# Kernel optimization log

Measured on AMD Instinct MI355X. Metric: run time of the kernel, lower is better.

## Reference

```python
import jax, jax.numpy as jnp
import numpy as np

VOCAB = 32000
EMB = 512
STATE = 512
B = 4
S = 1024


def setup_inputs() -> dict:
    key = jax.random.key(0)
    ks = jax.random.split(key, 6)
    x = jax.random.randint(ks[0], (B, S), 0, VOCAB)
    emb_table = jax.random.normal(ks[1], (VOCAB, EMB), dtype=jnp.float32)
    a = jax.random.normal(ks[2], (STATE, STATE), dtype=jnp.float32) * 0.02
    b = jax.random.normal(ks[3], (EMB, STATE), dtype=jnp.float32) * 0.02
    # nn.Linear(state, vocab): weight [vocab, state], bias [vocab]
    lim = 1.0 / np.sqrt(STATE)
    c_w = jax.random.uniform(ks[4], (VOCAB, STATE), minval=-lim, maxval=lim, dtype=jnp.float32)
    c_b = jax.random.uniform(ks[5], (VOCAB,), minval=-lim, maxval=lim, dtype=jnp.float32)
    return {"x": x, "emb_table": emb_table, "a": a, "b": b, "c_w": c_w, "c_b": c_b}


def reference(x, emb_table, a, b, c_w, c_b):
    emb = emb_table[x]                      # [B, S, E]
    # Precompute input projection for all timesteps (single GEMM).
    u = jnp.einsum('bse,en->bsn', emb, b)   # [B, S, N]
    u_t = jnp.swapaxes(u, 0, 1)             # [S, B, N] for scan

    def step(state, u_step):
        new_state = jnp.tanh(state @ a + u_step)  # [B, N]
        return new_state, new_state

    init = jnp.zeros((x.shape[0], a.shape[0]), dtype=emb.dtype)
    _, states = jax.lax.scan(step, init, u_t)   # states: [S, B, N]
    # Readout (dropout=0 -> identity). One big GEMM over all timesteps.
    logits = jnp.einsum('sbn,vn->sbv', states, c_w) + c_b  # [S, B, V]
    return jnp.swapaxes(logits, 0, 1)           # [B, S, V]
```

## Files before the change

### kernel.cpp

```cpp
#include <hip/hip_runtime.h>
#include <hip/hip_fp16.h>

typedef _Float16 f16;
typedef _Float16 f16x8 __attribute__((ext_vector_type(8)));
typedef _Float16 f16x4 __attribute__((ext_vector_type(4)));
typedef float f32x4v __attribute__((ext_vector_type(4)));
typedef unsigned long long u64;

#define S_LEN 1024
#define NS 512
#define NV 32000
#define NW 4
#define SENT 0x7C007C007C007C00ULL
#define FUSED_LDS 98304
#define TPB 896

#define MFMA16(a, b, c) __builtin_amdgcn_mfma_f32_16x16x32_f16((a), (b), (c), 0, 0, 0)

#define XLD(p) __hip_atomic_load((p), __ATOMIC_RELAXED, __HIP_MEMORY_SCOPE_AGENT)


__global__ __launch_bounds__(256) void transpose512_f16_kernel(
        const float* __restrict__ src, f16* __restrict__ dstT,
        u64* __restrict__ X) {
    int idx = blockIdx.x * 256 + threadIdx.x;
    X[idx] = SENT;
    X[idx + 262144] = SENT;
    int r = idx >> 9;
    int c = idx & 511;
    dstT[c * 512 + r] = (f16)src[idx];
}

__global__ __launch_bounds__(256) void embu_kernel(
        const int* __restrict__ x, const float* __restrict__ emb,
        const f16* __restrict__ bT, f16* __restrict__ u16) {
    __shared__ f16 embA[64 * 40];
    __shared__ f16 Bt[512 * 40];
    __shared__ int xi[64];

    int t = threadIdx.x;
    int wg = blockIdx.x;
    if (t < 64) {
        int m = wg * 64 + t;
        int bb = m & 3, ss = m >> 2;
        xi[t] = x[bb * S_LEN + ss];
    }
    __syncthreads();

    int wv = t >> 6, l = t & 63, lr = l & 15, lg = l >> 4;

    f32x4v acc[32];
#pragma unroll
    for (int i = 0; i < 32; i++) acc[i] = (f32x4v){0.f, 0.f, 0.f, 0.f};

    for (int kc = 0; kc < 512; kc += 32) {
        __syncthreads();
        {
            int tk = t >> 2, c0 = (t & 3) * 8;
            const float* src = emb + (size_t)xi[tk] * NS + kc + c0;
            float4 v0 = *(const float4*)src;
            float4 v1 = *(const float4*)(src + 4);
            f16x8 h;
            h[0] = (f16)v0.x; h[1] = (f16)v0.y; h[2] = (f16)v0.z; h[3] = (f16)v0.w;
            h[4] = (f16)v1.x; h[5] = (f16)v1.y; h[6] = (f16)v1.z; h[7] = (f16)v1.w;
            *(f16x8*)&embA[tk * 40 + c0] = h;
        }
        {
            int c0 = (t & 3) * 8;
            int n0 = t >> 2;
#pragma unroll
            for (int rr = 0; rr < 8; rr++) {
                int n = rr * 64 + n0;
                f16x8 v = *(const f16x8*)&bT[n * 512 + kc + c0];
                *(f16x8*)&Bt[n * 40 + c0] = v;
            }
        }
        __syncthreads();

        f16x8 af = *(const f16x8*)&embA[(wv * 16 + lr) * 40 + 8 * lg];
#pragma unroll
        for (int vt = 0; vt < 32; vt++) {
            f16x8 bf = *(const f16x8*)&Bt[(vt * 16 + lr) * 40 + 8 * lg];
            acc[vt] = MFMA16(af, bf, acc[vt]);
        }
    }

    int m0 = wg * 64 + wv * 16 + 4 * lg;
    int ss = m0 >> 2;
#pragma unroll
    for (int vt = 0; vt < 32; vt++) {
        int n = vt * 16 + lr;
        f16x4 h;
#pragma unroll
        for (int i = 0; i < 4; i++) h[i] = (f16)acc[vt][i];
        *(f16x4*)&u16[((size_t)ss * NS + n) * 4] = h;
    }
}

__global__ __launch_bounds__(TPB) void fused_kernel(
        const float* __restrict__ a, const f16* __restrict__ u16,
        const float* __restrict__ cw, const float* __restrict__ cb,
        u64* __restrict__ X, float* __restrict__ out) {
    extern __shared__ char smem[];
    int t = threadIdx.x;
    int bid = blockIdx.x;
    int w = t >> 6, l = t & 63, lr = l & 15, lg = l >> 4;

    if (bid < NW) {
        f16* Sb = (f16*)smem;
        int r = bid;

        for (int i = t; i < 2 * 4 * 544; i += TPB) Sb[i] = (f16)0.f;

        if (w < 8) {
            int col = r * 128 + w * 16 + lr;

            f16x8 afr[16];
#pragma unroll
            for (int ks = 0; ks < 16; ks++) {
                f16x8 h;
#pragma unroll
                for (int j = 0; j < 8; j++)
                    h[j] = (f16)a[(size_t)(ks * 32 + 8 * lg + j) * NS + col];
                afr[ks] = h;
            }

            f16x4 upf = *(const f16x4*)&u16[(size_t)col * 4];

            __syncthreads();

#pragma unroll 1
            for (int s = 0; s < S_LEN; s++) {
                int cur = s & 1, nxt = cur ^ 1;

                f32x4v acca, accb;
                acca[0] = (float)upf[0]; acca[1] = (float)upf[1];
                acca[2] = (float)upf[2]; acca[3] = (float)upf[3];
                accb = (f32x4v){0.f, 0.f, 0.f, 0.f};

                {
                    int sn = (s + 1 < S_LEN) ? s + 1 : S_LEN - 1;
                    upf = *(const f16x4*)&u16[((size_t)sn * NS + col) * 4];
                }

                const char* sb = (const char*)Sb + cur * 4352 +
                                 (lr & 3) * 1088 + lg * 16;
#pragma unroll
                for (int ks = 0; ks < 16; ks += 2) {
                    f16x8 s0 = *(const f16x8*)(sb + ks * 64);
                    f16x8 s1 = *(const f16x8*)(sb + ks * 64 + 64);
                    acca = MFMA16(s0, afr[ks], acca);
                    accb = MFMA16(s1, afr[ks + 1], accb);
                }

                if (lg == 0) {
                    union { u64 u; f16 h[4]; } pk;
#pragma unroll
                    for (int i = 0; i < 4; i++) {
                        float y = acca[i] + accb[i];
                        float e = __expf(2.0f * y);
                        float rc = __builtin_amdgcn_rcpf(e + 1.0f);
                        y = __builtin_fmaf(-2.0f, rc, 1.0f);
                        pk.h[i] = (f16)y;
                    }
                    __hip_atomic_store(&X[(size_t)s * NS + col], pk.u,
                                       __ATOMIC_RELAXED,
                                       __HIP_MEMORY_SCOPE_AGENT);
                    if (s < S_LEN - 1) {
#pragma unroll
                        for (int i = 0; i < 4; i++)
                            Sb[nxt * 2176 + i * 544 + col] = pk.h[i];
                    }
                }
                if (s == S_LEN - 1) break;

                asm volatile("s_waitcnt lgkmcnt(0)" ::: "memory");
                __builtin_amdgcn_s_barrier();
                __builtin_amdgcn_sched_barrier(0);
            }
        } else {
            int gw = w - 8;
            int cwk = gw + (gw >= 2 * r ? 2 : 0);
            int gcol = cwk * 64 + l;

            __syncthreads();

#pragma unroll 1
            for (int s = 0; s < S_LEN - 1; s++) {
                int nxt = (s & 1) ^ 1;
                const u64* p = &X[(size_t)s * NS + gcol];

                u64 v;
                u64 a0 = XLD(p), a1 = XLD(p), a2 = XLD(p), a3 = XLD(p);
                for (;;) {
                    if (a0 != SENT) { v = a0; break; }
                    a0 = XLD(p);
                    if (a1 != SENT) { v = a1; break; }
                    a1 = XLD(p);
                    if (a2 != SENT) { v = a2; break; }
                    a2 = XLD(p);
                    if (a3 != SENT) { v = a3; break; }
                    a3 = XLD(p);
                }
                __builtin_amdgcn_sched_barrier(0);

                union { u64 u; f16 h[4]; } pk;
                pk.u = v;
#pragma unroll
                for (int i = 0; i < 4; i++)
                    Sb[nxt * 2176 + i * 544 + gcol] = pk.h[i];

                asm volatile("s_waitcnt lgkmcnt(0)" ::: "memory");
                __builtin_amdgcn_s_barrier();
                __builtin_amdgcn_sched_barrier(0);
            }
        }
        return;
    }

    char* AstB = smem;
    char* BwB  = smem + 256 * 64 * 2;

    int idx = bid - NW;
    int bm = idx / 250;
    int bn = idx % 250;
    int s0 = bm * 64;

    if (t == 0) {
        int sc = s0 + 56;
        while (XLD(&X[(size_t)sc * NS]) == SENT)
            __builtin_amdgcn_s_sleep(16);
    }
    __syncthreads();

    int wr = w >> 1, wc = w & 1;

    f32x4v acc[4][4];
#pragma unroll
    for (int i = 0; i < 4; i++)
#pragma unroll
        for (int j = 0; j < 4; j++) acc[i][j] = (f32x4v){0.f, 0.f, 0.f, 0.f};

    for (int kc = 0; kc < 512; kc += 64) {
        __syncthreads();
        if (t < 512) {
            {
                int srel = t >> 3;
                int ck = (t & 7) * 8;
                const u64* xs = &X[(size_t)(s0 + srel) * NS + kc + ck];
                u64 v[8];
#pragma unroll
                for (int j = 0; j < 8; j++) v[j] = xs[j];
#pragma unroll
                for (int j = 0; j < 8; j++)
                    while (v[j] == SENT) v[j] = XLD(&xs[j]);
#pragma unroll
                for (int b = 0; b < 4; b++) {
                    f16x8 row;
#pragma unroll
                    for (int j = 0; j < 8; j++) {
                        union { u64 u; f16 h[4]; } pk;
                        pk.u = v[j];
                        row[j] = pk.h[b];
                    }
                    int rr = srel * 4 + b;
                    int byte = (rr * 128 + ck * 2) ^ ((rr & 7) << 4);
                    *(f16x8*)(AstB + byte) = row;
                }
            }
#pragma unroll
            for (int q = 0; q < 4; q++) {
                int i2 = q * 512 + t;
                int row = i2 >> 4;
                int c0 = (i2 & 15) * 4;
                float4 v = *(const float4*)&cw[(size_t)(bn * 128 + row) * NS +
                                               kc + c0];
                f16x4 h;
                h[0] = (f16)v.x; h[1] = (f16)v.y; h[2] = (f16)v.z; h[3] = (f16)v.w;
                int byte = (row * 128 + c0 * 2) ^ ((row & 7) << 4);
                *(f16x4*)(BwB + byte) = h;
            }
        }
        __syncthreads();

        if (w < 8) {
#pragma unroll
            for (int ks = 0; ks < 2; ks++) {
                f16x8 af[4], bf[4];
#pragma unroll
                for (int mt = 0; mt < 4; mt++) {
                    int rr = wr * 64 + mt * 16 + lr;
                    int byte = (rr * 128 + ks * 64 + lg * 16) ^ ((lr & 7) << 4);
                    af[mt] = *(const f16x8*)(AstB + byte);
                }
#pragma unroll
                for (int vt = 0; vt < 4; vt++) {
                    int rr = wc * 64 + vt * 16 + lr;
                    int byte = (rr * 128 + ks * 64 + lg * 16) ^ ((lr & 7) << 4);
                    bf[vt] = *(const f16x8*)(BwB + byte);
                }
#pragma unroll
                for (int mt = 0; mt < 4; mt++)
#pragma unroll
                    for (int vt = 0; vt < 4; vt++)
                        acc[mt][vt] = MFMA16(af[mt], bf[vt], acc[mt][vt]);
            }
        }
    }

    if (w < 8) {
        float bias[4];
#pragma unroll
        for (int vt = 0; vt < 4; vt++)
            bias[vt] = cb[bn * 128 + wc * 64 + vt * 16 + lr];

#pragma unroll
        for (int mt = 0; mt < 4; mt++) {
#pragma unroll
            for (int i = 0; i < 4; i++) {
                int m = bm * 256 + wr * 64 + mt * 16 + 4 * lg + i;
                int bb = m & 3, ss = m >> 2;
                float* orow = out + (size_t)(bb * S_LEN + ss) * NV +
                              bn * 128 + wc * 64;
#pragma unroll
                for (int vt = 0; vt < 4; vt++)
                    orow[vt * 16 + lr] = acc[mt][vt][i] + bias[vt];
            }
        }
    }
}

extern "C" void kernel_launch(void* const* d_in, const int* in_sizes, int n_in,
                              void* d_out, int out_size, void* d_ws, size_t ws_size,
                              hipStream_t stream) {
    (void)in_sizes; (void)n_in; (void)out_size; (void)ws_size;

    const int*   x   = (const int*)d_in[0];
    const float* emb = (const float*)d_in[1];
    const float* a   = (const float*)d_in[2];
    const float* bm  = (const float*)d_in[3];
    const float* cw  = (const float*)d_in[4];
    const float* cb  = (const float*)d_in[5];
    float* out = (float*)d_out;

    char* ws = (char*)d_ws;
    f16* u16 = (f16*)(ws);
    u64* X   = (u64*)(ws + (4u << 20));
    f16* bT16 = (f16*)(ws + (8u << 20));

    hipFuncSetAttribute(reinterpret_cast<const void*>(fused_kernel),
                        hipFuncAttributeMaxDynamicSharedMemorySize,
                        FUSED_LDS);

    transpose512_f16_kernel<<<1024, 256, 0, stream>>>(bm, bT16, X);
    embu_kernel<<<64, 256, 0, stream>>>(x, emb, bT16, u16);
    fused_kernel<<<NW + 16 * 250, TPB, FUSED_LDS, stream>>>(
        a, u16, cw, cb, X, out);
}
```

Before: 1.462 ms.

## Shrink fused kernel to 512 threads and merge gather role into compute waves

The block size drops from 896 to 512 threads. The dedicated gather waves (waves 8-13) of the recurrence blocks are removed, so six of the eight compute waves now also poll the global X buffer for other blocks' state columns after each step. The GEMM blocks no longer carry six idle waves, which can raise occupancy and register budget per thread. The cost is that polling now sits on the critical path of the compute waves in the serial recurrence, which could lengthen every step.

Measured after the change: 1.486 ms. Within noise of the previous version (+1.6%).

```diff
diff --git a/kernel.cpp b/kernel.cpp
--- a/kernel.cpp
+++ b/kernel.cpp
@@ -13,7 +13,6 @@
 #define NW 4
 #define SENT 0x7C007C007C007C00ULL
 #define FUSED_LDS 98304
-#define TPB 896
 
 #define MFMA16(a, b, c) __builtin_amdgcn_mfma_f32_16x16x32_f16((a), (b), (c), 0, 0, 0)
 
@@ -97,7 +96,7 @@
     }
 }
 
-__global__ __launch_bounds__(TPB) void fused_kernel(
+__global__ __launch_bounds__(512) void fused_kernel(
         const float* __restrict__ a, const f16* __restrict__ u16,
         const float* __restrict__ cw, const float* __restrict__ cb,
         u64* __restrict__ X, float* __restrict__ out) {
@@ -109,87 +108,75 @@
     if (bid < NW) {
         f16* Sb = (f16*)smem;
         int r = bid;
-
-        for (int i = t; i < 2 * 4 * 544; i += TPB) Sb[i] = (f16)0.f;
-
-        if (w < 8) {
-            int col = r * 128 + w * 16 + lr;
-
-            f16x8 afr[16];
-#pragma unroll
-            for (int ks = 0; ks < 16; ks++) {
-                f16x8 h;
-#pragma unroll
-                for (int j = 0; j < 8; j++)
-                    h[j] = (f16)a[(size_t)(ks * 32 + 8 * lg + j) * NS + col];
-                afr[ks] = h;
-            }
-
-            f16x4 upf = *(const f16x4*)&u16[(size_t)col * 4];
-
-            __syncthreads();
+        int col = r * 128 + w * 16 + lr;
+
+        int gcol = -1;
+        if (w < 6) {
+            int cwk = w + (w >= 2 * r ? 2 : 0);
+            gcol = cwk * 64 + l;
+        }
+
+        for (int i = t; i < 2 * 4 * 544; i += 512) Sb[i] = (f16)0.f;
+
+        f16x8 afr[16];
+#pragma unroll
+        for (int ks = 0; ks < 16; ks++) {
+            f16x8 h;
+#pragma unroll
+            for (int j = 0; j < 8; j++)
+                h[j] = (f16)a[(size_t)(ks * 32 + 8 * lg + j) * NS + col];
+            afr[ks] = h;
+        }
+
+        f16x4 upf = *(const f16x4*)&u16[(size_t)col * 4];
+
+        __syncthreads();
 
 #pragma unroll 1
-            for (int s = 0; s < S_LEN; s++) {
-                int cur = s & 1, nxt = cur ^ 1;
-
-                f32x4v acca, accb;
-                acca[0] = (float)upf[0]; acca[1] = (float)upf[1];
-                acca[2] = (float)upf[2]; acca[3] = (float)upf[3];
-                accb = (f32x4v){0.f, 0.f, 0.f, 0.f};
-
-                {
-                    int sn = (s + 1 < S_LEN) ? s + 1 : S_LEN - 1;
-                    upf = *(const f16x4*)&u16[((size_t)sn * NS + col) * 4];
+        for (int s = 0; s < S_LEN; s++) {
+            int cur = s & 1, nxt = cur ^ 1;
+
+            f32x4v acca, accb;
+            acca[0] = (float)upf[0]; acca[1] = (float)upf[1];
+            acca[2] = (float)upf[2]; acca[3] = (float)upf[3];
+            accb = (f32x4v){0.f, 0.f, 0.f, 0.f};
+
+            {
+                int sn = (s + 1 < S_LEN) ? s + 1 : S_LEN - 1;
+                upf = *(const f16x4*)&u16[((size_t)sn * NS + col) * 4];
+            }
+
+            const char* sb = (const char*)Sb + cur * 4352 +
+                             (lr & 3) * 1088 + lg * 16;
+#pragma unroll
+            for (int ks = 0; ks < 16; ks += 2) {
+                f16x8 s0 = *(const f16x8*)(sb + ks * 64);
+                f16x8 s1 = *(const f16x8*)(sb + ks * 64 + 64);
+                acca = MFMA16(s0, afr[ks], acca);
+                accb = MFMA16(s1, afr[ks + 1], accb);
+            }
+
+            if (lg == 0) {
+                union { u64 u; f16 h[4]; } pk;
+#pragma unroll
+                for (int i = 0; i < 4; i++) {
+                    float y = acca[i] + accb[i];
+                    float e = __expf(2.0f * y);
+                    float rc = __builtin_amdgcn_rcpf(e + 1.0f);
+                    y = __builtin_fmaf(-2.0f, rc, 1.0f);
+                    pk.h[i] = (f16)y;
                 }
-
-                const char* sb = (const char*)Sb + cur * 4352 +
-                                 (lr & 3) * 1088 + lg * 16;
-#pragma unroll
-                for (int ks = 0; ks < 16; ks += 2) {
-                    f16x8 s0 = *(const f16x8*)(sb + ks * 64);
-                    f16x8 s1 = *(const f16x8*)(sb + ks * 64 + 64);
-                    acca = MFMA16(s0, afr[ks], acca);
-                    accb = MFMA16(s1, afr[ks + 1], accb);
-                }
-
-                if (lg == 0) {
-                    union { u64 u; f16 h[4]; } pk;
-#pragma unroll
-                    for (int i = 0; i < 4; i++) {
-                        float y = acca[i] + accb[i];
-                        float e = __expf(2.0f * y);
-                        float rc = __builtin_amdgcn_rcpf(e + 1.0f);
-                        y = __builtin_fmaf(-2.0f, rc, 1.0f);
-                        pk.h[i] = (f16)y;
-                    }
-                    __hip_atomic_store(&X[(size_t)s * NS + col], pk.u,
-                                       __ATOMIC_RELAXED,
-                                       __HIP_MEMORY_SCOPE_AGENT);
-                    if (s < S_LEN - 1) {
-#pragma unroll
-                        for (int i = 0; i < 4; i++)
-                            Sb[nxt * 2176 + i * 544 + col] = pk.h[i];
-                    }
-                }
-                if (s == S_LEN - 1) break;
-
-                asm volatile("s_waitcnt lgkmcnt(0)" ::: "memory");
-                __builtin_amdgcn_s_barrier();
-                __builtin_amdgcn_sched_barrier(0);
-            }
-        } else {
-            int gw = w - 8;
-            int cwk = gw + (gw >= 2 * r ? 2 : 0);
-            int gcol = cwk * 64 + l;
-
-            __syncthreads();
-
-#pragma unroll 1
-            for (int s = 0; s < S_LEN - 1; s++) {
-                int nxt = (s & 1) ^ 1;
+                __hip_atomic_store(&X[(size_t)s * NS + col], pk.u,
+                                   __ATOMIC_RELAXED, __HIP_MEMORY_SCOPE_AGENT);
+#pragma unroll
+                for (int i = 0; i < 4; i++)
+                    Sb[nxt * 2176 + i * 544 + col] = pk.h[i];
+            }
+
+            if (s == S_LEN - 1) break;
+
+            if (w < 6) {
                 const u64* p = &X[(size_t)s * NS + gcol];
-
                 u64 v;
                 u64 a0 = XLD(p), a1 = XLD(p), a2 = XLD(p), a3 = XLD(p);
                 for (;;) {
@@ -202,18 +189,16 @@
                     if (a3 != SENT) { v = a3; break; }
                     a3 = XLD(p);
                 }
-                __builtin_amdgcn_sched_barrier(0);
-
                 union { u64 u; f16 h[4]; } pk;
                 pk.u = v;
 #pragma unroll
                 for (int i = 0; i < 4; i++)
                     Sb[nxt * 2176 + i * 544 + gcol] = pk.h[i];
-
-                asm volatile("s_waitcnt lgkmcnt(0)" ::: "memory");
-                __builtin_amdgcn_s_barrier();
-                __builtin_amdgcn_sched_barrier(0);
-            }
+            }
+
+            asm volatile("s_waitcnt lgkmcnt(0)" ::: "memory");
+            __builtin_amdgcn_s_barrier();
+            __builtin_amdgcn_sched_barrier(0);
         }
         return;
     }
@@ -243,89 +228,81 @@
 
     for (int kc = 0; kc < 512; kc += 64) {
         __syncthreads();
-        if (t < 512) {
-            {
-                int srel = t >> 3;
-                int ck = (t & 7) * 8;
-                const u64* xs = &X[(size_t)(s0 + srel) * NS + kc + ck];
-                u64 v[8];
-#pragma unroll
-                for (int j = 0; j < 8; j++) v[j] = xs[j];
-#pragma unroll
-                for (int j = 0; j < 8; j++)
-                    while (v[j] == SENT) v[j] = XLD(&xs[j]);
-#pragma unroll
-                for (int b = 0; b < 4; b++) {
-                    f16x8 row;
-#pragma unroll
-                    for (int j = 0; j < 8; j++) {
-                        union { u64 u; f16 h[4]; } pk;
-                        pk.u = v[j];
-                        row[j] = pk.h[b];
-                    }
-                    int rr = srel * 4 + b;
-                    int byte = (rr * 128 + ck * 2) ^ ((rr & 7) << 4);
-                    *(f16x8*)(AstB + byte) = row;
+        {
+            int srel = t >> 3;
+            int ck = (t & 7) * 8;
+            const u64* xs = &X[(size_t)(s0 + srel) * NS + kc + ck];
+            u64 v[8];
+#pragma unroll
+            for (int j = 0; j < 8; j++) v[j] = xs[j];
+#pragma unroll
+            for (int j = 0; j < 8; j++)
+                while (v[j] == SENT) v[j] = XLD(&xs[j]);
+#pragma unroll
+            for (int b = 0; b < 4; b++) {
+                f16x8 row;
+#pragma unroll
+                for (int j = 0; j < 8; j++) {
+                    union { u64 u; f16 h[4]; } pk;
+                    pk.u = v[j];
+                    row[j] = pk.h[b];
                 }
-            }
-#pragma unroll
-            for (int q = 0; q < 4; q++) {
-                int i2 = q * 512 + t;
-                int row = i2 >> 4;
-                int c0 = (i2 & 15) * 4;
-                float4 v = *(const float4*)&cw[(size_t)(bn * 128 + row) * NS +
-                                               kc + c0];
-                f16x4 h;
-                h[0] = (f16)v.x; h[1] = (f16)v.y; h[2] = (f16)v.z; h[3] = (f16)v.w;
-                int byte = (row * 128 + c0 * 2) ^ ((row & 7) << 4);
-                *(f16x4*)(BwB + byte) = h;
-            }
-        }
-        __syncthreads();
-
-        if (w < 8) {
-#pragma unroll
-            for (int ks = 0; ks < 2; ks++) {
-                f16x8 af[4], bf[4];
-#pragma unroll
-                for (int mt = 0; mt < 4; mt++) {
-                    int rr = wr * 64 + mt * 16 + lr;
-                    int byte = (rr * 128 + ks * 64 + lg * 16) ^ ((lr & 7) << 4);
-                    af[mt] = *(const f16x8*)(AstB + byte);
-                }
-#pragma unroll
-                for (int vt = 0; vt < 4; vt++) {
-                    int rr = wc * 64 + vt * 16 + lr;
-                    int byte = (rr * 128 + ks * 64 + lg * 16) ^ ((lr & 7) << 4);
-                    bf[vt] = *(const f16x8*)(BwB + byte);
-                }
-#pragma unroll
-                for (int mt = 0; mt < 4; mt++)
-#pragma unroll
-                    for (int vt = 0; vt < 4; vt++)
-                        acc[mt][vt] = MFMA16(af[mt], bf[vt], acc[mt][vt]);
-            }
-        }
-    }
-
-    if (w < 8) {
-        float bias[4];
-#pragma unroll
-        for (int vt = 0; vt < 4; vt++)
-            bias[vt] = cb[bn * 128 + wc * 64 + vt * 16 + lr];
-
-#pragma unroll
-        for (int mt = 0; mt < 4; mt++) {
-#pragma unroll
-            for (int i = 0; i < 4; i++) {
-                int m = bm * 256 + wr * 64 + mt * 16 + 4 * lg + i;
-                int bb = m & 3, ss = m >> 2;
-                float* orow = out + (size_t)(bb * S_LEN + ss) * NV +
-                              bn * 128 + wc * 64;
+                int rr = srel * 4 + b;
+                int byte = (rr * 128 + ck * 2) ^ ((rr & 7) << 4);
+                *(f16x8*)(AstB + byte) = row;
+            }
+        }
+#pragma unroll
+        for (int q = 0; q < 4; q++) {
+            int i2 = q * 512 + t;
+            int row = i2 >> 4;
+            int c0 = (i2 & 15) * 4;
+            float4 v = *(const float4*)&cw[(size_t)(bn * 128 + row) * NS + kc + c0];
+            f16x4 h;
+            h[0] = (f16)v.x; h[1] = (f16)v.y; h[2] = (f16)v.z; h[3] = (f16)v.w;
+            int byte = (row * 128 + c0 * 2) ^ ((row & 7) << 4);
+            *(f16x4*)(BwB + byte) = h;
+        }
+        __syncthreads();
+
+#pragma unroll
+        for (int ks = 0; ks < 2; ks++) {
+            f16x8 af[4], bf[4];
+#pragma unroll
+            for (int mt = 0; mt < 4; mt++) {
+                int rr = wr * 64 + mt * 16 + lr;
+                int byte = (rr * 128 + ks * 64 + lg * 16) ^ ((lr & 7) << 4);
+                af[mt] = *(const f16x8*)(AstB + byte);
+            }
+#pragma unroll
+            for (int vt = 0; vt < 4; vt++) {
+                int rr = wc * 64 + vt * 16 + lr;
+                int byte = (rr * 128 + ks * 64 + lg * 16) ^ ((lr & 7) << 4);
+                bf[vt] = *(const f16x8*)(BwB + byte);
+            }
+#pragma unroll
+            for (int mt = 0; mt < 4; mt++)
 #pragma unroll
                 for (int vt = 0; vt < 4; vt++)
-                    orow[vt * 16 + lr] = acc[mt][vt][i] + bias[vt];
-            }
+                    acc[mt][vt] = MFMA16(af[mt], bf[vt], acc[mt][vt]);
+        }
+    }
+
+    float bias[4];
+#pragma unroll
+    for (int vt = 0; vt < 4; vt++)
+        bias[vt] = cb[bn * 128 + wc * 64 + vt * 16 + lr];
+
+#pragma unroll
+    for (int mt = 0; mt < 4; mt++) {
+#pragma unroll
+        for (int i = 0; i < 4; i++) {
+            int m = bm * 256 + wr * 64 + mt * 16 + 4 * lg + i;
+            int bb = m & 3, ss = m >> 2;
+            float* orow = out + (size_t)(bb * S_LEN + ss) * NV + bn * 128 + wc * 64;
+#pragma unroll
+            for (int vt = 0; vt < 4; vt++)
+                orow[vt * 16 + lr] = acc[mt][vt][i] + bias[vt];
         }
     }
 }
@@ -354,6 +331,6 @@
 
     transpose512_f16_kernel<<<1024, 256, 0, stream>>>(bm, bT16, X);
     embu_kernel<<<64, 256, 0, stream>>>(x, emb, bT16, u16);
-    fused_kernel<<<NW + 16 * 250, TPB, FUSED_LDS, stream>>>(
+    fused_kernel<<<NW + 16 * 250, 512, FUSED_LDS, stream>>>(
         a, u16, cw, cb, X, out);
 }
```
